# Optimization experiments

Hardware: AMD Instinct MI355X
Metric: run time of the kernel (lower is better)

The kernel has to match this reference:

```python
import jax, jax.numpy as jnp
import numpy as np

NUM_HEADS = 16


def setup_inputs() -> dict:
    key = jax.random.key(0)
    k1, k2, k3, k4 = jax.random.split(key, 4)
    B, N, C = 4, 1024, 1024
    x = jax.random.normal(k1, (B, N, C), dtype=jnp.float32)
    mask = jnp.ones((B, N), dtype=jnp.float32)  # 1 = visible token
    # 0.02 init scale keeps logits in a sane range (avoids saturated softmax)
    W_qkv = jax.random.normal(k2, (C, 3 * C), dtype=jnp.float32) * 0.02
    W_proj = jax.random.normal(k3, (C, C), dtype=jnp.float32) * 0.02
    b_proj = jax.random.normal(k4, (C,), dtype=jnp.float32) * 0.02
    return {"x": x, "mask": mask, "W_qkv": W_qkv, "W_proj": W_proj, "b_proj": b_proj}


def reference(x, mask, W_qkv, W_proj, b_proj):
    B, N, C = x.shape
    H = NUM_HEADS
    D = C // H
    scale = D ** -0.5
    qkv = (x @ W_qkv).reshape(B, N, 3, H, D)
    q, k, v = qkv[:, :, 0], qkv[:, :, 1], qkv[:, :, 2]  # each [B, N, H, D]
    attn = jnp.einsum("bnhd,bmhd->bhnm", q, k) * scale  # [B, H, N, N]
    attn = attn + (1.0 - mask)[:, None, None, :] * -5.0  # additive mask penalty
    attn = jax.nn.softmax(attn, axis=-1)
    out = jnp.einsum("bhnm,bmhd->bnhd", attn, v).reshape(B, N, C)
    return out @ W_proj + b_proj
```

## Files before the change

kernel.cpp:

```cpp
#include <hip/hip_runtime.h>

typedef __attribute__((ext_vector_type(8))) short bf16x8;
typedef __attribute__((ext_vector_type(4))) float f32x4;
typedef __attribute__((ext_vector_type(16))) float f32x16;
typedef __attribute__((ext_vector_type(4))) float fl4;
typedef __attribute__((ext_vector_type(8))) unsigned short u16x8;
typedef __attribute__((ext_vector_type(4))) unsigned short u16x4;
typedef __attribute__((ext_vector_type(2))) int i32x2;
typedef __attribute__((ext_vector_type(4))) int i32x4;

#define MFMA16(A,B,C) __builtin_amdgcn_mfma_f32_16x16x32_bf16((A),(B),(C),0,0,0)
#define MFMA32(A,B,C) __builtin_amdgcn_mfma_f32_32x32x16_bf16((A),(B),(C),0,0,0)

__device__ __forceinline__ unsigned short f2bf_bits(float x) {
  union { float f; unsigned u; } v; v.f = x;
  unsigned r = v.u + 0x7fffu + ((v.u >> 16) & 1u);
  return (unsigned short)(r >> 16);
}

__device__ __forceinline__ void gload_lds16(const void* g, void* l) {
  __builtin_amdgcn_global_load_lds((const __attribute__((address_space(1))) void*)g,
                                   (__attribute__((address_space(3))) void*)l, 16, 0, 0);
}

__device__ __forceinline__ bf16x8 lds_frag(const char* base, int row, int bir) {
  int off = (row << 7) + bir;
  off ^= (row & 7) << 4;
  return *(const bf16x8*)(base + off);
}

__device__ __forceinline__ int cvtpk_bf16(float a, float b) {
  int r; asm("v_cvt_pk_bf16_f32 %0, %1, %2" : "=v"(r) : "v"(a), "v"(b)); return r;
}

__device__ __forceinline__ void plswap(int& a, int& b) {
#if __has_builtin(__builtin_amdgcn_permlane32_swap)
  i32x2 r = __builtin_amdgcn_permlane32_swap(a, b, false, false);
  a = r[0]; b = r[1];
#else
  asm volatile("s_nop 1\n\tv_permlane32_swap_b32 %0, %1" : "+v"(a), "+v"(b));
#endif
}

__global__ __launch_bounds__(256) void k_cvt(const float* __restrict__ src,
                                             unsigned short* __restrict__ dst, int n) {
  int i = (blockIdx.x * 256 + threadIdx.x) * 8;
  if (i >= n) return;
  fl4 a = *(const fl4*)(src + i);
  fl4 b = *(const fl4*)(src + i + 4);
  u16x8 o;
  o[0] = f2bf_bits(a[0]); o[1] = f2bf_bits(a[1]); o[2] = f2bf_bits(a[2]); o[3] = f2bf_bits(a[3]);
  o[4] = f2bf_bits(b[0]); o[5] = f2bf_bits(b[1]); o[6] = f2bf_bits(b[2]); o[7] = f2bf_bits(b[3]);
  *(u16x8*)(dst + i) = o;
}

__global__ __launch_bounds__(256) void k_tcvt2(const float* __restrict__ wqkv,
                                               unsigned short* __restrict__ dqkv,
                                               const float* __restrict__ wproj,
                                               unsigned short* __restrict__ dproj) {
  __shared__ float tile[64][65];
  const int bx = blockIdx.x;
  const float* src; unsigned short* dst; int NCOL, nt;
  if (bx < 48) { src = wqkv; dst = dqkv; NCOL = 3072; nt = bx * 64; }
  else         { src = wproj; dst = dproj; NCOL = 1024; nt = (bx - 48) * 64; }
  const int kt = blockIdx.y * 64;
  const int t = threadIdx.x;
  {
    int r = t >> 2, c0 = (t & 3) * 16;
    const float* s = src + (size_t)(kt + r) * NCOL + nt + c0;
    #pragma unroll
    for (int j = 0; j < 4; ++j) {
      fl4 v = *(const fl4*)(s + j * 4);
      tile[r][c0 + j * 4 + 0] = v[0]; tile[r][c0 + j * 4 + 1] = v[1];
      tile[r][c0 + j * 4 + 2] = v[2]; tile[r][c0 + j * 4 + 3] = v[3];
    }
  }
  __syncthreads();
  {
    int n = t >> 2, kc = (t & 3) * 16;
    unsigned short* d = dst + (size_t)(nt + n) * 1024 + kt + kc;
    u16x8 o0, o1;
    #pragma unroll
    for (int j = 0; j < 8; ++j) o0[j] = f2bf_bits(tile[kc + j][n]);
    #pragma unroll
    for (int j = 0; j < 8; ++j) o1[j] = f2bf_bits(tile[kc + 8 + j][n]);
    *(u16x8*)d = o0;
    *(u16x8*)(d + 8) = o1;
  }
}

template <int MODE>
__global__ __launch_bounds__(256) void k_gemm(const unsigned short* __restrict__ A,
                                              const unsigned short* __restrict__ Bt,
                                              unsigned short* __restrict__ qp,
                                              unsigned short* __restrict__ kp,
                                              unsigned short* __restrict__ vtp,
                                              const float* __restrict__ bias,
                                              float* __restrict__ outp) {
  __shared__ char lA[16384], lB[16384];
  const int tid = threadIdx.x, lane = tid & 63, w = tid >> 6;
  const int wm = w >> 1, wn = w & 1;
  const int m0 = blockIdx.y * 128, n0 = blockIdx.x * 128;
  const char* Ab = (const char*)A + (size_t)m0 * 2048;
  const char* Bb = (const char*)Bt + (size_t)n0 * 2048;

  f32x4 acc[4][4];
  #pragma unroll
  for (int mi = 0; mi < 4; ++mi)
    #pragma unroll
    for (int ni = 0; ni < 4; ++ni) acc[mi][ni] = f32x4{0.f, 0.f, 0.f, 0.f};

  for (int kt = 0; kt < 16; ++kt) {
    #pragma unroll
    for (int i = 0; i < 4; ++i) {
      int c = i * 256 + tid;
      int row = c >> 3, cc = c & 7, ccs = cc ^ (row & 7);
      char* dstA = lA + (i * 256 + w * 64) * 16;
      char* dstB = lB + (i * 256 + w * 64) * 16;
      gload_lds16(Ab + (size_t)row * 2048 + kt * 128 + ccs * 16, dstA);
      gload_lds16(Bb + (size_t)row * 2048 + kt * 128 + ccs * 16, dstB);
    }
    __syncthreads();
    #pragma unroll
    for (int ks = 0; ks < 2; ++ks) {
      bf16x8 af[4], bfv[4];
      #pragma unroll
      for (int mi = 0; mi < 4; ++mi)
        af[mi] = lds_frag(lA, wm * 64 + mi * 16 + (lane & 15), ks * 64 + ((lane >> 4) << 4));
      #pragma unroll
      for (int ni = 0; ni < 4; ++ni)
        bfv[ni] = lds_frag(lB, wn * 64 + ni * 16 + (lane & 15), ks * 64 + ((lane >> 4) << 4));
      #pragma unroll
      for (int mi = 0; mi < 4; ++mi)
        #pragma unroll
        for (int ni = 0; ni < 4; ++ni)
          acc[mi][ni] = MFMA16(af[mi], bfv[ni], acc[mi][ni]);
    }
    __syncthreads();
  }

  if (MODE == 0) {
    #pragma unroll
    for (int mi = 0; mi < 4; ++mi) {
      int row0 = m0 + wm * 64 + mi * 16 + ((lane >> 4) << 2);
      int bb = row0 >> 10, nn0 = row0 & 1023;
      #pragma unroll
      for (int ni = 0; ni < 4; ++ni) {
        int col = n0 + wn * 64 + ni * 16 + (lane & 15);
        int tt = col >> 10, rem = col & 1023, h = rem >> 6, d = rem & 63;
        f32x4 a = acc[mi][ni];
        if (tt == 2) {
          u16x4 pv;
          pv[0] = f2bf_bits(a[0]); pv[1] = f2bf_bits(a[1]);
          pv[2] = f2bf_bits(a[2]); pv[3] = f2bf_bits(a[3]);
          *(u16x4*)(vtp + (((size_t)(bb * 16 + h) * 64 + d) << 10) + nn0) = pv;
        } else {
          unsigned short* dst = (tt == 0) ? qp : kp;
          size_t base = ((size_t)(bb * 16 + h)) << 16;
          #pragma unroll
          for (int r = 0; r < 4; ++r)
            dst[base + (size_t)(nn0 + r) * 64 + d] = f2bf_bits(a[r]);
        }
      }
    }
  } else {
    #pragma unroll
    for (int mi = 0; mi < 4; ++mi) {
      int row0 = m0 + wm * 64 + mi * 16 + ((lane >> 4) << 2);
      #pragma unroll
      for (int ni = 0; ni < 4; ++ni) {
        int col = n0 + wn * 64 + ni * 16 + (lane & 15);
        float bv = bias[col];
        f32x4 a = acc[mi][ni];
        #pragma unroll
        for (int r = 0; r < 4; ++r)
          outp[(size_t)(row0 + r) * 1024 + col] = a[r] + bv;
      }
    }
  }
}

__global__ __launch_bounds__(256, 4) void k_attn(const unsigned short* __restrict__ qp,
                                                 const unsigned short* __restrict__ kp,
                                                 const unsigned short* __restrict__ vtp,
                                                 const float* __restrict__ mask,
                                                 unsigned short* __restrict__ aop) {
  __shared__ __align__(16) char lds[32768];
  const int tid = threadIdx.x, lane = tid & 63, w = tid >> 6;
  const int hi = lane >> 5, lq = lane & 31;
  const int pair = w >> 1;
  const int g = blockIdx.x;
  const int bh = (g & 7) * 8 + (g >> 7);
  const int qc = (g >> 3) & 15;
  const int b = bh >> 4, h = bh & 15;
  const char* kb = (const char*)(kp + ((size_t)bh << 16));
  const char* vb = (const char*)(vtp + ((size_t)bh << 16));
  const unsigned short* qh = qp + ((size_t)bh << 16);
  const float* mrow = mask + b * 1024 + pair * 512;
  const int q0 = qc * 64 + (w & 1) * 32;

  const int krow = tid >> 3, kslot = tid & 7;
  const int kcc = kslot ^ (krow & 7);
  const char* gKA = kb + (size_t)krow * 128 + kcc * 16;
  const char* gKB = gKA + 512 * 128;
  const int vrow = tid >> 2, vslot = tid & 3;
  const int vcc = vslot ^ ((vrow >> 1) & 3);
  const char* gVA = vb + (size_t)vrow * 2048 + vcc * 16;
  const char* gVB = gVA + 512 * 2;
  char* const dK = lds + tid * 16;
  char* const dV = lds + 8192 + tid * 16;

  const char* const myK = lds + pair * 4096;
  const char* const myV = lds + 8192 + pair * 4096;
  int kfo[4], vfo[4];
  #pragma unroll
  for (int dc = 0; dc < 4; ++dc)
    kfo[dc] = lq * 128 + (((dc << 1) | hi) ^ (lq & 7)) * 16;
  #pragma unroll
  for (int ks = 0; ks < 2; ++ks)
    #pragma unroll
    for (int nb = 0; nb < 2; ++nb) {
      int row = nb * 32 + lq;
      vfo[ks * 2 + nb] = row * 64 + (((ks << 1) | hi) ^ ((row >> 1) & 3)) * 16;
    }

  int bws[16];
  #pragma unroll
  for (int t2 = 0; t2 < 16; ++t2) {
    float mv = mrow[t2 * 32 + lq];
    bws[t2] = (hi == 0) ? (int)f2bf_bits((1.0f - mv) * -40.0f) : 0;
  }

  bf16x8 qB[4];
  #pragma unroll
  for (int dc = 0; dc < 4; ++dc)
    qB[dc] = *(const bf16x8*)(qh + (q0 + lq) * 64 + dc * 16 + hi * 8);

  i32x4 onesw = {hi == 0 ? 0x3F80 : 0, 0, 0, 0};
  const bf16x8 onesB = __builtin_bit_cast(bf16x8, onesw);

  f32x16 O0, O1;
  #pragma unroll
  for (int i = 0; i < 16; ++i) { O0[i] = 0.f; O1[i] = 0.f; }
  float lsum = 0.f;

#define STAGE(BUF, T)                                                          \
  do {                                                                         \
    gload_lds16(gKA + (T) * 4096, dK + (BUF) * 16384);                         \
    gload_lds16(gKB + (T) * 4096, dK + (BUF) * 16384 + 4096);                  \
    gload_lds16(gVA + (T) * 64,   dV + (BUF) * 16384);                         \
    gload_lds16(gVB + (T) * 64,   dV + (BUF) * 16384 + 4096);                  \
  } while (0)

#define STEP(BUF, T, LAST)                                                     \
  do {                                                                         \
    if (!(LAST)) STAGE((BUF) ^ 1, (T) + 1);                                    \
    const char* K = myK + (BUF) * 16384;                                       \
    const char* V = myV + (BUF) * 16384;                                       \
    f32x16 acc;                                                                \
    _Pragma("unroll") for (int i = 0; i < 16; ++i) acc[i] = 0.f;               \
    __builtin_amdgcn_s_setprio(1);                                             \
    _Pragma("unroll") for (int dc = 0; dc < 4; ++dc) {                         \
      bf16x8 kf = *(const bf16x8*)(K + kfo[dc]);                               \
      acc = MFMA32(kf, qB[dc], acc);                                           \
    }                                                                          \
    __builtin_amdgcn_s_setprio(0);                                             \
    {                                                                          \
      i32x4 bwv = {bws[T], 0, 0, 0};                                           \
      acc = MFMA32(__builtin_bit_cast(bf16x8, bwv), onesB, acc);               \
    }                                                                          \
    float p[16];                                                               \
    _Pragma("unroll") for (int r = 0; r < 16; ++r) {                           \
      p[r] = exp2f(fmaf(acc[r], 0.18033688f, -5.7707802f));                    \
      lsum += p[r];                                                            \
    }                                                                          \
    int X0 = cvtpk_bf16(p[0], p[1]),   X1 = cvtpk_bf16(p[2], p[3]);            \
    int Y0 = cvtpk_bf16(p[4], p[5]),   Y1 = cvtpk_bf16(p[6], p[7]);            \
    int Z0 = cvtpk_bf16(p[8], p[9]),   Z1 = cvtpk_bf16(p[10], p[11]);          \
    int W0 = cvtpk_bf16(p[12], p[13]), W1 = cvtpk_bf16(p[14], p[15]);          \
    plswap(X0, Y0); plswap(X1, Y1);                                            \
    plswap(Z0, W0); plswap(Z1, W1);                                            \
    i32x4 pa0v = {X0, X1, Y0, Y1};                                             \
    i32x4 pa1v = {Z0, Z1, W0, W1};                                             \
    const bf16x8 PA0 = __builtin_bit_cast(bf16x8, pa0v);                       \
    const bf16x8 PA1 = __builtin_bit_cast(bf16x8, pa1v);                       \
    bf16x8 va0 = *(const bf16x8*)(V + vfo[0]);                                 \
    bf16x8 va1 = *(const bf16x8*)(V + vfo[1]);                                 \
    bf16x8 vb0 = *(const bf16x8*)(V + vfo[2]);                                 \
    bf16x8 vb1 = *(const bf16x8*)(V + vfo[3]);                                 \
    __builtin_amdgcn_s_setprio(1);                                             \
    O0 = MFMA32(PA0, va0, O0);                                                 \
    O1 = MFMA32(PA0, va1, O1);                                                 \
    O0 = MFMA32(PA1, vb0, O0);                                                 \
    O1 = MFMA32(PA1, vb1, O1);                                                 \
    __builtin_amdgcn_s_setprio(0);                                             \
    __syncthreads();                                                           \
  } while (0)

  STAGE(0, 0);
  __syncthreads();
  #pragma unroll
  for (int tt = 0; tt < 8; ++tt) {
    STEP(0, 2 * tt, 0);
    STEP(1, 2 * tt + 1, tt == 7);
  }
#undef STEP
#undef STAGE

  float tot = lsum + __shfl_xor(lsum, 32);
  float* fx = (float*)lds;
  if (pair == 1) {
    int base = (w - 2) * 64 * 34 + lane * 34;
    #pragma unroll
    for (int r = 0; r < 16; ++r) { fx[base + r] = O0[r]; fx[base + 16 + r] = O1[r]; }
    fx[base + 32] = tot;
  }
  __syncthreads();
  if (pair == 0) {
    int base = w * 64 * 34 + lane * 34;
    float invT = 1.0f / (tot + fx[base + 32]);
    #pragma unroll
    for (int r = 0; r < 16; ++r) {
      int qr = (r & 3) + 8 * (r >> 2) + 4 * hi;
      float iv = __shfl(invT, qr);
      float o0 = (O0[r] + fx[base + r]) * iv;
      float o1 = (O1[r] + fx[base + 16 + r]) * iv;
      size_t ob = (size_t)(b * 1024 + q0 + qr) * 1024 + h * 64 + lq;
      aop[ob] = f2bf_bits(o0);
      aop[ob + 32] = f2bf_bits(o1);
    }
  }
}

extern "C" void kernel_launch(void* const* d_in, const int* in_sizes, int n_in,
                              void* d_out, int out_size, void* d_ws, size_t ws_size,
                              hipStream_t stream) {
  const float* x     = (const float*)d_in[0];
  const float* mask  = (const float*)d_in[1];
  const float* wqkv  = (const float*)d_in[2];
  const float* wproj = (const float*)d_in[3];
  const float* bproj = (const float*)d_in[4];
  float* out = (float*)d_out;

  char* ws = (char*)d_ws;
  unsigned short* xb     = (unsigned short*)(ws);
  unsigned short* wqkvt  = (unsigned short*)(ws + 8388608);
  unsigned short* wprojt = (unsigned short*)(ws + 14680064);
  unsigned short* qbuf   = (unsigned short*)(ws + 16777216);
  unsigned short* kbuf   = (unsigned short*)(ws + 25165824);
  unsigned short* vtbuf  = (unsigned short*)(ws + 33554432);
  unsigned short* aobuf  = (unsigned short*)(ws + 41943040);

  k_cvt<<<dim3(2048), dim3(256), 0, stream>>>(x, xb, 4194304);
  k_tcvt2<<<dim3(64, 16), dim3(256), 0, stream>>>(wqkv, wqkvt, wproj, wprojt);
  k_gemm<0><<<dim3(24, 32), dim3(256), 0, stream>>>(xb, wqkvt, qbuf, kbuf, vtbuf, nullptr, nullptr);
  k_attn<<<dim3(1024), dim3(256), 0, stream>>>(qbuf, kbuf, vtbuf, mask, aobuf);
  k_gemm<1><<<dim3(8, 32), dim3(256), 0, stream>>>(aobuf, wprojt, nullptr, nullptr, nullptr, bproj, out);
}
```

Measured before the change: 106.2 us.

## Double attention block to 128 queries and triple-buffer K/V with vmcnt waits

The attention kernel now runs 512-thread blocks that each handle 128 queries, so every K/V tile staged into LDS is reused by twice as many waves and global K/V traffic per query is halved. The two-stage buffer with a trailing `__syncthreads` becomes a three-stage LDS ring. Each step waits with `s_waitcnt vmcnt` and a single barrier before prefetching two tiles ahead, which is meant to hide load latency better. In exchange the block needs 48KB of LDS and the launch bounds tighten, which may cut occupancy or raise register pressure, and there are half as many blocks to spread across the CUs.

Result: no change. 105.8 us (-0.4%).

```diff
diff --git a/kernel.cpp b/kernel.cpp
--- a/kernel.cpp
+++ b/kernel.cpp
@@ -180,38 +180,34 @@
   }
 }
 
-__global__ __launch_bounds__(256, 4) void k_attn(const unsigned short* __restrict__ qp,
+__global__ __launch_bounds__(512, 4) void k_attn(const unsigned short* __restrict__ qp,
                                                  const unsigned short* __restrict__ kp,
                                                  const unsigned short* __restrict__ vtp,
                                                  const float* __restrict__ mask,
                                                  unsigned short* __restrict__ aop) {
-  __shared__ __align__(16) char lds[32768];
+  __shared__ __align__(16) char lds[49152];
   const int tid = threadIdx.x, lane = tid & 63, w = tid >> 6;
   const int hi = lane >> 5, lq = lane & 31;
-  const int pair = w >> 1;
+  const int pair = w >> 2, qsub = w & 3;
   const int g = blockIdx.x;
-  const int bh = (g & 7) * 8 + (g >> 7);
-  const int qc = (g >> 3) & 15;
+  const int bh = (g & 7) * 8 + ((g >> 6) & 7);
+  const int qc = (g >> 3) & 7;
   const int b = bh >> 4, h = bh & 15;
   const char* kb = (const char*)(kp + ((size_t)bh << 16));
   const char* vb = (const char*)(vtp + ((size_t)bh << 16));
   const unsigned short* qh = qp + ((size_t)bh << 16);
   const float* mrow = mask + b * 1024 + pair * 512;
-  const int q0 = qc * 64 + (w & 1) * 32;
-
-  const int krow = tid >> 3, kslot = tid & 7;
-  const int kcc = kslot ^ (krow & 7);
-  const char* gKA = kb + (size_t)krow * 128 + kcc * 16;
-  const char* gKB = gKA + 512 * 128;
-  const int vrow = tid >> 2, vslot = tid & 3;
-  const int vcc = vslot ^ ((vrow >> 1) & 3);
-  const char* gVA = vb + (size_t)vrow * 2048 + vcc * 16;
-  const char* gVB = gVA + 512 * 2;
+  const int q0 = qc * 128 + qsub * 32;
+
+  const int kpk = tid >> 8, krow = (tid >> 3) & 31, kslot = tid & 7;
+  const char* gK = kb + (size_t)kpk * 65536 + (size_t)krow * 128
+                   + ((kslot ^ (krow & 7)) * 16);
+  const int vpk = tid >> 8, vrow = (tid >> 2) & 63, vslot = tid & 3;
+  const char* gV = vb + (size_t)vpk * 1024 + (size_t)vrow * 2048
+                   + ((vslot ^ ((vrow >> 1) & 3)) * 16);
   char* const dK = lds + tid * 16;
   char* const dV = lds + 8192 + tid * 16;
 
-  const char* const myK = lds + pair * 4096;
-  const char* const myV = lds + 8192 + pair * 4096;
   int kfo[4], vfo[4];
   #pragma unroll
   for (int dc = 0; dc < 4; ++dc)
@@ -246,17 +242,19 @@
 
 #define STAGE(BUF, T)                                                          \
   do {                                                                         \
-    gload_lds16(gKA + (T) * 4096, dK + (BUF) * 16384);                         \
-    gload_lds16(gKB + (T) * 4096, dK + (BUF) * 16384 + 4096);                  \
-    gload_lds16(gVA + (T) * 64,   dV + (BUF) * 16384);                         \
-    gload_lds16(gVB + (T) * 64,   dV + (BUF) * 16384 + 4096);                  \
+    gload_lds16(gK + (T) * 4096, dK + (BUF) * 16384);                          \
+    gload_lds16(gV + (T) * 64,   dV + (BUF) * 16384);                          \
   } while (0)
 
-#define STEP(BUF, T, LAST)                                                     \
+#define VMCNT(N) asm volatile("s_waitcnt vmcnt(" #N ")" ::: "memory")
+
+#define STEP(BUF, T, N)                                                        \
   do {                                                                         \
-    if (!(LAST)) STAGE((BUF) ^ 1, (T) + 1);                                    \
-    const char* K = myK + (BUF) * 16384;                                       \
-    const char* V = myV + (BUF) * 16384;                                       \
+    VMCNT(N);                                                                  \
+    __builtin_amdgcn_s_barrier();                                              \
+    if ((T) + 2 <= 15) STAGE(((T) + 2) % 3, (T) + 2);                          \
+    const char* K = lds + (BUF) * 16384 + pair * 4096;                         \
+    const char* V = lds + (BUF) * 16384 + 8192 + pair * 4096;                  \
     f32x16 acc;                                                                \
     _Pragma("unroll") for (int i = 0; i < 16; ++i) acc[i] = 0.f;               \
     __builtin_amdgcn_s_setprio(1);                                             \
@@ -294,30 +292,30 @@
     O0 = MFMA32(PA1, vb0, O0);                                                 \
     O1 = MFMA32(PA1, vb1, O1);                                                 \
     __builtin_amdgcn_s_setprio(0);                                             \
-    __syncthreads();                                                           \
   } while (0)
 
   STAGE(0, 0);
+  STAGE(1, 1);
+  STEP(0, 0, 2);  STEP(1, 1, 2);  STEP(2, 2, 2);  STEP(0, 3, 2);
+  STEP(1, 4, 2);  STEP(2, 5, 2);  STEP(0, 6, 2);  STEP(1, 7, 2);
+  STEP(2, 8, 2);  STEP(0, 9, 2);  STEP(1, 10, 2); STEP(2, 11, 2);
+  STEP(0, 12, 2); STEP(1, 13, 2); STEP(2, 14, 2); STEP(0, 15, 0);
+#undef STEP
+#undef VMCNT
+#undef STAGE
+
   __syncthreads();
-  #pragma unroll
-  for (int tt = 0; tt < 8; ++tt) {
-    STEP(0, 2 * tt, 0);
-    STEP(1, 2 * tt + 1, tt == 7);
-  }
-#undef STEP
-#undef STAGE
-
   float tot = lsum + __shfl_xor(lsum, 32);
   float* fx = (float*)lds;
   if (pair == 1) {
-    int base = (w - 2) * 64 * 34 + lane * 34;
+    int base = qsub * 64 * 34 + lane * 34;
     #pragma unroll
     for (int r = 0; r < 16; ++r) { fx[base + r] = O0[r]; fx[base + 16 + r] = O1[r]; }
     fx[base + 32] = tot;
   }
   __syncthreads();
   if (pair == 0) {
-    int base = w * 64 * 34 + lane * 34;
+    int base = qsub * 64 * 34 + lane * 34;
     float invT = 1.0f / (tot + fx[base + 32]);
     #pragma unroll
     for (int r = 0; r < 16; ++r) {
@@ -354,6 +352,6 @@
   k_cvt<<<dim3(2048), dim3(256), 0, stream>>>(x, xb, 4194304);
   k_tcvt2<<<dim3(64, 16), dim3(256), 0, stream>>>(wqkv, wqkvt, wproj, wprojt);
   k_gemm<0><<<dim3(24, 32), dim3(256), 0, stream>>>(xb, wqkvt, qbuf, kbuf, vtbuf, nullptr, nullptr);
-  k_attn<<<dim3(1024), dim3(256), 0, stream>>>(qbuf, kbuf, vtbuf, mask, aobuf);
+  k_attn<<<dim3(512), dim3(512), 0, stream>>>(qbuf, kbuf, vtbuf, mask, aobuf);
   k_gemm<1><<<dim3(8, 32), dim3(256), 0, stream>>>(aobuf, wprojt, nullptr, nullptr, nullptr, bproj, out);
 }
```
